# Kernel optimization log

Measured on AMD Instinct MI355X. Metric: run time of the kernel, lower is better.

The kernel has to match this reference:

```python
import jax, jax.numpy as jnp
import numpy as np

IN_C = 64
OUT_C = 128
HEADS = 8
DIM = 9 * IN_C  # 576


def unfold3x3_s2(fea):
    # torch.nn.functional.unfold(fea, (3,3), padding=1, stride=2)
    # returns [N, C*9, L] with channel-major (c, kh, kw) ordering.
    N, C, H, W = fea.shape
    Ho, Wo = H // 2, W // 2
    p = jnp.pad(fea, ((0, 0), (0, 0), (1, 1), (1, 1)))
    patches = jnp.stack(
        [p[:, :, ki:ki + 2 * Ho:2, kj:kj + 2 * Wo:2] for ki in range(3) for kj in range(3)],
        axis=2,
    )  # [N, C, 9, Ho, Wo]
    return patches.reshape(N, C * 9, Ho * Wo)


def mhsa(x, w_qkv, b_qkv, w_out, b_out):
    # standard ViT attention: x [B, L, D]
    B, L, D = x.shape
    dh = D // HEADS
    qkv = x @ w_qkv + b_qkv  # [B, L, 3D]
    q, k, v = jnp.split(qkv, 3, axis=-1)
    def heads(t):
        return t.reshape(B, L, HEADS, dh).transpose(0, 2, 1, 3)  # [B, h, L, dh]
    q, k, v = heads(q), heads(k), heads(v)
    scale = dh ** -0.5
    scores = jnp.einsum('bhqd,bhkd->bhqk', q, k) * scale
    attn = jax.nn.softmax(scores, axis=-1)
    o = jnp.einsum('bhqk,bhkd->bhqd', attn, v)  # [B, h, L, dh]
    o = o.transpose(0, 2, 1, 3).reshape(B, L, D)
    return o @ w_out + b_out


def setup_inputs() -> dict:
    key = jax.random.key(0)
    ks = jax.random.split(key, 6)
    s = DIM ** -0.5
    return {
        'fea': jax.random.normal(ks[0], (1, IN_C, 128, 128), dtype=jnp.float32),
        'w_qkv': jax.random.normal(ks[1], (DIM, 3 * DIM), dtype=jnp.float32) * s,
        'b_qkv': jnp.zeros((3 * DIM,), dtype=jnp.float32),
        'w_out': jax.random.normal(ks[2], (DIM, DIM), dtype=jnp.float32) * s,
        'b_out': jnp.zeros((DIM,), dtype=jnp.float32),
        'conv_w': jax.random.normal(ks[3], (OUT_C, IN_C, 3, 3), dtype=jnp.float32) * s,
    }


def reference(fea, w_qkv, b_qkv, w_out, b_out, conv_w):
    N, C, H, W = fea.shape
    Ho, Wo = H // 2, W // 2
    x = unfold3x3_s2(fea).transpose(0, 2, 1)          # [N, L, 9C]
    x = mhsa(x, w_qkv, b_qkv, w_out, b_out) + x       # residual
    # matmul with reshaped conv weights: [N, L, 9C] @ [9C, out_c]
    y = x @ conv_w.reshape(OUT_C, -1).T               # [N, L, out_c]
    y = y.transpose(0, 2, 1).reshape(N, OUT_C, Ho, Wo)  # fold with (1,1) kernel
    return jax.nn.silu(y)
```

## Files before the change

### kernel.cpp

```cpp
#include <hip/hip_runtime.h>
#include <hip/hip_bf16.h>
#include <math.h>

#define L_TOK 4096
#define D_DIM 576
#define NHEADS 8
#define DHEAD 72
#define DPAD 96
#define HSZ ((size_t)NHEADS * L_TOK * DPAD)
#define KSPLIT 4
#define LOG2E 1.4426950408889634f

typedef __attribute__((ext_vector_type(8))) short short8;
typedef __attribute__((ext_vector_type(4))) short short4v;
typedef __attribute__((ext_vector_type(4))) float float4v;

union F4S8 {
  float4 f4;
  short8 s8;
  __hip_bfloat16 h[8];
};

__device__ inline void tc_body(const float* __restrict__ src,
                               __hip_bfloat16* __restrict__ dst, int R, int C,
                               int bi, int bj, int t, __hip_bfloat16* Ts) {
  const int col = t & 63, row4 = t >> 6;
#pragma unroll
  for (int u = 0; u < 16; u++) {
    int r = u * 4 + row4;
    Ts[r * 68 + col] = __float2bfloat16(src[(size_t)(bj * 64 + r) * C + bi * 64 + col]);
  }
  __syncthreads();
#pragma unroll
  for (int u = 0; u < 16; u++) {
    int c = u * 4 + row4;
    dst[(size_t)(bi * 64 + c) * R + bj * 64 + col] = Ts[col * 68 + c];
  }
}

__global__ __launch_bounds__(256) void prep_all(const float* __restrict__ fea,
                                                const float* __restrict__ w_qkv,
                                                const float* __restrict__ w_out,
                                                const float* __restrict__ conv_w,
                                                __hip_bfloat16* __restrict__ xb,
                                                __hip_bfloat16* __restrict__ WqkvT,
                                                __hip_bfloat16* __restrict__ WoT,
                                                __hip_bfloat16* __restrict__ CwB) {
  __shared__ float Shm[3120];
  const int b = blockIdx.x;
  const int t = threadIdx.x;
  if (b < 512) {
    float* Lf = Shm;
    const int ho = b & 63;
    const int c0 = (b >> 6) * 8;
    for (int e = t; e < 3072; e += 256) {
      int c = e / 384;
      int rr = (e / 128) % 3;
      int w = e & 127;
      int h = 2 * ho + rr - 1;
      float v = 0.f;
      if ((unsigned)h < 128u) v = fea[(size_t)(c0 + c) * 16384 + h * 128 + w];
      Lf[(c * 3 + rr) * 130 + w + 1] = v;
    }
    if (t < 24) { Lf[t * 130] = 0.f; Lf[t * 130 + 129] = 0.f; }
    __syncthreads();
    for (int e = t; e < 576; e += 256) {
      int wo = e / 9, ch = e - wo * 9;
      F4S8 u;
#pragma unroll
      for (int j = 0; j < 8; j++) {
        int dd = ch * 8 + j;
        int c = dd / 9, k = dd - c * 9;
        int ki = k / 3, kj = k - ki * 3;
        u.h[j] = __float2bfloat16(Lf[(c * 3 + ki) * 130 + 2 * wo + kj]);
      }
      *(float4*)(xb + (size_t)(ho * 64 + wo) * D_DIM + c0 * 9 + ch * 8) = u.f4;
    }
  } else if (b < 755) {
    int bb = b - 512;
    tc_body(w_qkv, WqkvT, D_DIM, 1728, bb % 27, bb / 27, t, (__hip_bfloat16*)Shm);
  } else if (b < 836) {
    int bb = b - 755;
    tc_body(w_out, WoT, D_DIM, D_DIM, bb % 9, bb / 9, t, (__hip_bfloat16*)Shm);
  } else {
    int i = (b - 836) * 256 + t;
    CwB[i] = __float2bfloat16(conv_w[i]);
  }
}

template <int EPI, int NMI>
__global__ __launch_bounds__(256) void gemm_mfma(const __hip_bfloat16* __restrict__ A,
                                                 const __hip_bfloat16* __restrict__ Bt,
                                                 const float* __restrict__ bias,
                                                 const __hip_bfloat16* __restrict__ resid,
                                                 __hip_bfloat16* __restrict__ outB,
                                                 __hip_bfloat16* __restrict__ outB2) {
  constexpr int K = D_DIM;
  constexpr int BM = NMI * 32;
  __shared__ __align__(16) __hip_bfloat16 As[BM * 72];
  __shared__ __align__(16) __hip_bfloat16 Bs[64 * 72];
  const int t = threadIdx.x;
  const int wave = t >> 6, lane = t & 63, quad = lane >> 4, l16 = lane & 15;
  const int wm = (wave & 2) * (NMI * 8);
  const int wn = (wave & 1) * 32;
  const int m0 = blockIdx.x * BM, n0 = blockIdx.y * 64;

  float4v acc[NMI][2];
#pragma unroll
  for (int i = 0; i < NMI; i++)
#pragma unroll
    for (int j = 0; j < 2; j++) acc[i][j] = (float4v){0.f, 0.f, 0.f, 0.f};

  const int arow = t >> 3, ach = t & 7;
  for (int k0 = 0; k0 < K; k0 += 64) {
    __syncthreads();
#pragma unroll
    for (int u = 0; u < NMI; u++) {
      int row = u * 32 + arow;
      *(float4*)(&As[row * 72 + ach * 8]) =
          *(const float4*)(A + (size_t)(m0 + row) * K + k0 + ach * 8);
    }
#pragma unroll
    for (int u = 0; u < 2; u++) {
      int row = u * 32 + arow;
      *(float4*)(&Bs[row * 72 + ach * 8]) =
          *(const float4*)(Bt + (size_t)(n0 + row) * K + k0 + ach * 8);
    }
    __syncthreads();
    short8 af[NMI][2], bfr[2][2];
#pragma unroll
    for (int i = 0; i < NMI; i++)
#pragma unroll
      for (int s = 0; s < 2; s++)
        af[i][s] = *(const short8*)(&As[(wm + i * 16 + l16) * 72 + s * 32 + quad * 8]);
#pragma unroll
    for (int j = 0; j < 2; j++)
#pragma unroll
      for (int s = 0; s < 2; s++)
        bfr[j][s] = *(const short8*)(&Bs[(wn + j * 16 + l16) * 72 + s * 32 + quad * 8]);
#pragma unroll
    for (int i = 0; i < NMI; i++)
#pragma unroll
      for (int j = 0; j < 2; j++) {
        acc[i][j] = __builtin_amdgcn_mfma_f32_16x16x32_bf16(af[i][0], bfr[j][0], acc[i][j], 0, 0, 0);
        acc[i][j] = __builtin_amdgcn_mfma_f32_16x16x32_bf16(af[i][1], bfr[j][1], acc[i][j], 0, 0, 0);
      }
  }

  if (EPI == 0) {
    const int part = n0 / D_DIM;
    if (part < 2) {
      __hip_bfloat16* dst = outB + (size_t)part * HSZ;
#pragma unroll
      for (int j = 0; j < 2; j++) {
        int ng = n0 + wn + j * 16 + l16;
        float bv = bias[ng];
        int rem = ng - part * D_DIM;
        int h = rem / DHEAD;
        int d = rem - h * DHEAD;
#pragma unroll
        for (int i = 0; i < NMI; i++) {
          int mb = m0 + wm + i * 16 + quad * 4;
#pragma unroll
          for (int r = 0; r < 4; r++)
            dst[((size_t)h * L_TOK + mb + r) * DPAD + d] = __float2bfloat16(acc[i][j][r] + bv);
        }
      }
    } else {
      __hip_bfloat16* Ls = As;
      __syncthreads();
      const int n0rel = n0 - 2 * D_DIM;
#pragma unroll
      for (int j = 0; j < 2; j++) {
        int nloc = wn + j * 16 + l16;
        float bv = bias[n0 + nloc];
#pragma unroll
        for (int i = 0; i < NMI; i++) {
          int mloc = wm + i * 16 + quad * 4;
#pragma unroll
          for (int r = 0; r < 4; r++)
            Ls[nloc * 136 + mloc + r] = __float2bfloat16(acc[i][j][r] + bv);
        }
      }
      __syncthreads();
      for (int e = t; e < 1024; e += 256) {
        int row = e >> 4, ch = e & 15;
        int ng = n0rel + row;
        int hh = ng / DHEAD, dd = ng - hh * DHEAD;
        *(float4*)(outB2 + ((size_t)hh * DPAD + dd) * L_TOK + m0 + ch * 8) =
            *(const float4*)(&Ls[row * 136 + ch * 8]);
      }
    }
  } else {
#pragma unroll
    for (int j = 0; j < 2; j++) {
      int ng = n0 + wn + j * 16 + l16;
      float bv = bias[ng];
#pragma unroll
      for (int i = 0; i < NMI; i++) {
        int mb = m0 + wm + i * 16 + quad * 4;
#pragma unroll
        for (int r = 0; r < 4; r++) {
          size_t idx = (size_t)(mb + r) * D_DIM + ng;
          float v = acc[i][j][r] + bv + __bfloat162float(resid[idx]);
          outB[idx] = __float2bfloat16(v);
        }
      }
    }
  }
}

__global__ __launch_bounds__(256) void final_small(const __hip_bfloat16* __restrict__ A,
                                                   const __hip_bfloat16* __restrict__ Bt,
                                                   float* __restrict__ out) {
  __shared__ __align__(16) __hip_bfloat16 As[32 * 72];
  __shared__ __align__(16) __hip_bfloat16 Bs[32 * 72];
  const int t = threadIdx.x;
  const int wave = t >> 6, lane = t & 63, quad = lane >> 4, l16 = lane & 15;
  const int wm = (wave & 2) * 8;
  const int wn = (wave & 1) * 16;
  const int m0 = blockIdx.x * 32, n0 = blockIdx.y * 32;

  float4v acc = (float4v){0.f, 0.f, 0.f, 0.f};

  const int arow = t >> 3, ach = t & 7;
  for (int k0 = 0; k0 < D_DIM; k0 += 64) {
    __syncthreads();
    *(float4*)(&As[arow * 72 + ach * 8]) =
        *(const float4*)(A + (size_t)(m0 + arow) * D_DIM + k0 + ach * 8);
    *(float4*)(&Bs[arow * 72 + ach * 8]) =
        *(const float4*)(Bt + (size_t)(n0 + arow) * D_DIM + k0 + ach * 8);
    __syncthreads();
    short8 af[2], bfr[2];
#pragma unroll
    for (int s = 0; s < 2; s++) {
      af[s] = *(const short8*)(&As[(wm + l16) * 72 + s * 32 + quad * 8]);
      bfr[s] = *(const short8*)(&Bs[(wn + l16) * 72 + s * 32 + quad * 8]);
    }
    acc = __builtin_amdgcn_mfma_f32_16x16x32_bf16(af[0], bfr[0], acc, 0, 0, 0);
    acc = __builtin_amdgcn_mfma_f32_16x16x32_bf16(af[1], bfr[1], acc, 0, 0, 0);
  }
  const int oc = n0 + wn + l16;
  const int mb = m0 + wm + quad * 4;
#pragma unroll
  for (int r = 0; r < 4; r++) {
    float v = acc[r];
    float sg = 1.f / (1.f + __expf(-v));
    out[(size_t)oc * L_TOK + mb + r] = v * sg;
  }
}

#define KS_STRIDE 104
#define VT_STRIDE 72
#define PS_STRIDE 72

__global__ __launch_bounds__(256, 2) void attn_mfma(const __hip_bfloat16* __restrict__ Qb,
                                                    const __hip_bfloat16* __restrict__ Kb,
                                                    const __hip_bfloat16* __restrict__ VbT,
                                                    __hip_bfloat16* __restrict__ Opart,
                                                    float* __restrict__ Ml) {
  __shared__ __align__(16) __hip_bfloat16 Ks[64 * KS_STRIDE];
  __shared__ __align__(16) __hip_bfloat16 Vt[80 * VT_STRIDE];
  __shared__ __align__(16) __hip_bfloat16 Ps[4 * 64 * PS_STRIDE];

  const int bid = blockIdx.x;
  const int h = bid & 7;
  const int rest = bid >> 3;
  const int ksp = rest & 3;
  const int qblk = rest >> 2;
  const int t = threadIdx.x;
  const int wave = t >> 6;
  const int lane = t & 63;
  const int quad = lane >> 4;
  const int l16 = lane & 15;

  const __hip_bfloat16* Qh = Qb + (size_t)h * L_TOK * DPAD;
  const __hip_bfloat16* Kh = Kb + (size_t)h * L_TOK * DPAD;
  const __hip_bfloat16* VhT = VbT + (size_t)h * DPAD * L_TOK;

  const int qbase = qblk * 256 + wave * 64;
  short8 qf[4][3];
#pragma unroll
  for (int mi = 0; mi < 4; mi++) {
#pragma unroll
    for (int s = 0; s < 3; s++) {
      if (s == 2 && quad >= 1) {
        qf[mi][s] = (short8){0, 0, 0, 0, 0, 0, 0, 0};
      } else {
        qf[mi][s] = *(const short8*)(Qh + (size_t)(qbase + mi * 16 + l16) * DPAD + s * 32 + quad * 8);
      }
    }
  }

  const float4 zero4 = {0.f, 0.f, 0.f, 0.f};
  if (t < 192) {
    int row = t / 3, ch = 9 + t % 3;
    *(float4*)(&Ks[row * KS_STRIDE + ch * 8]) = zero4;
  }
  if (t >= 192) {
    int e = t - 192;
    int d = 72 + (e >> 3), ch = e & 7;
    *(float4*)(&Vt[d * VT_STRIDE + ch * 8]) = zero4;
  }

  float4v Of[4][5];
#pragma unroll
  for (int mi = 0; mi < 4; mi++)
#pragma unroll
    for (int nt = 0; nt < 5; nt++) Of[mi][nt] = (float4v){0.f, 0.f, 0.f, 0.f};
  float mrow[4] = {-INFINITY, -INFINITY, -INFINITY, -INFINITY};
  float lrow[4] = {0.f, 0.f, 0.f, 0.f};
  const float scale2 = 0.11785113019775792f * LOG2E;

  __hip_bfloat16* myPs = Ps + wave * 64 * PS_STRIDE;
  const int kstart = ksp * 1024;

  for (int kt = 0; kt < 16; kt++) {
    const int kbase = kstart + kt * 64;
    __syncthreads();

    for (int e = t; e < 576; e += 256) {
      int row = e / 9, ch = e - row * 9;
      *(float4*)(&Ks[row * KS_STRIDE + ch * 8]) =
          *(const float4*)(Kh + (size_t)(kbase + row) * DPAD + ch * 8);
    }
    for (int e = t; e < 576; e += 256) {
      int d = e >> 3, ch = e & 7;
      *(float4*)(&Vt[d * VT_STRIDE + ch * 8]) =
          *(const float4*)(VhT + (size_t)d * L_TOK + kbase + ch * 8);
    }
    __syncthreads();

    float4v S[4][4];
#pragma unroll
    for (int ks = 0; ks < 4; ks++) {
      float4v a0 = (float4v){0.f, 0.f, 0.f, 0.f};
      float4v a1 = a0, a2 = a0, a3 = a0;
#pragma unroll
      for (int s = 0; s < 3; s++) {
        short8 kf = *(const short8*)(&Ks[(ks * 16 + l16) * KS_STRIDE + s * 32 + quad * 8]);
        a0 = __builtin_amdgcn_mfma_f32_16x16x32_bf16(kf, qf[0][s], a0, 0, 0, 0);
        a1 = __builtin_amdgcn_mfma_f32_16x16x32_bf16(kf, qf[1][s], a1, 0, 0, 0);
        a2 = __builtin_amdgcn_mfma_f32_16x16x32_bf16(kf, qf[2][s], a2, 0, 0, 0);
        a3 = __builtin_amdgcn_mfma_f32_16x16x32_bf16(kf, qf[3][s], a3, 0, 0, 0);
      }
#pragma unroll
      for (int r = 0; r < 4; r++) {
        S[0][ks][r] = a0[r]; S[1][ks][r] = a1[r];
        S[2][ks][r] = a2[r]; S[3][ks][r] = a3[r];
      }
    }

    float alpha[4];
#pragma unroll
    for (int mi = 0; mi < 4; mi++) {
      float tm = -INFINITY;
#pragma unroll
      for (int ks = 0; ks < 4; ks++)
#pragma unroll
        for (int r = 0; r < 4; r++) tm = fmaxf(tm, S[mi][ks][r]);
      tm = fmaxf(tm, __shfl_xor(tm, 16));
      tm = fmaxf(tm, __shfl_xor(tm, 32));
      float mnew = fmaxf(mrow[mi], tm * scale2);
      alpha[mi] = exp2f(mrow[mi] - mnew);
      mrow[mi] = mnew;
      float ps = 0.f;
#pragma unroll
      for (int ks = 0; ks < 4; ks++)
#pragma unroll
        for (int r = 0; r < 4; r++) {
          float p = exp2f(fmaf(S[mi][ks][r], scale2, -mnew));
          ps += p;
          S[mi][ks][r] = p;
        }
      ps += __shfl_xor(ps, 16);
      ps += __shfl_xor(ps, 32);
      lrow[mi] = lrow[mi] * alpha[mi] + ps;
    }

#pragma unroll
    for (int mi = 0; mi < 4; mi++) {
#pragma unroll
      for (int ks = 0; ks < 4; ks++) {
        union { short4v v; __hip_bfloat16 hh[4]; } pk;
#pragma unroll
        for (int r = 0; r < 4; r++) pk.hh[r] = __float2bfloat16(S[mi][ks][r]);
        *(short4v*)(&myPs[(mi * 16 + l16) * PS_STRIDE + ks * 16 + quad * 4]) = pk.v;
      }
    }

    {
      float aq[4][4];
#pragma unroll
      for (int mi = 0; mi < 4; mi++)
#pragma unroll
        for (int r = 0; r < 4; r++) aq[mi][r] = __shfl(alpha[mi], quad * 4 + r);
#pragma unroll
      for (int mi = 0; mi < 4; mi++)
#pragma unroll
        for (int nt = 0; nt < 5; nt++)
#pragma unroll
          for (int r = 0; r < 4; r++) Of[mi][nt][r] *= aq[mi][r];
    }

#pragma unroll
    for (int kstep = 0; kstep < 2; kstep++) {
      short8 pa[4];
#pragma unroll
      for (int mi = 0; mi < 4; mi++)
        pa[mi] = *(const short8*)(&myPs[(mi * 16 + l16) * PS_STRIDE + kstep * 32 + quad * 8]);
#pragma unroll
      for (int nt = 0; nt < 5; nt++) {
        short8 vb = *(const short8*)(&Vt[(nt * 16 + l16) * VT_STRIDE + kstep * 32 + quad * 8]);
        Of[0][nt] = __builtin_amdgcn_mfma_f32_16x16x32_bf16(pa[0], vb, Of[0][nt], 0, 0, 0);
        Of[1][nt] = __builtin_amdgcn_mfma_f32_16x16x32_bf16(pa[1], vb, Of[1][nt], 0, 0, 0);
        Of[2][nt] = __builtin_amdgcn_mfma_f32_16x16x32_bf16(pa[2], vb, Of[2][nt], 0, 0, 0);
        Of[3][nt] = __builtin_amdgcn_mfma_f32_16x16x32_bf16(pa[3], vb, Of[3][nt], 0, 0, 0);
      }
    }
  }

  const size_t pb = ((size_t)ksp * NHEADS + h) * L_TOK;
#pragma unroll
  for (int mi = 0; mi < 4; mi++) {
#pragma unroll
    for (int nt = 0; nt < 5; nt++) {
      int d = nt * 16 + l16;
      if (d < DHEAD) {
#pragma unroll
        for (int r = 0; r < 4; r++) {
          int q = qbase + mi * 16 + quad * 4 + r;
          Opart[(pb + q) * 72 + d] = __float2bfloat16(Of[mi][nt][r]);
        }
      }
    }
  }
  if (quad == 0) {
#pragma unroll
    for (int mi = 0; mi < 4; mi++) {
      int q = qbase + mi * 16 + l16;
      Ml[(pb + q) * 2] = mrow[mi];
      Ml[(pb + q) * 2 + 1] = lrow[mi];
    }
  }
}

__global__ __launch_bounds__(256) void attn_merge(const __hip_bfloat16* __restrict__ Opart,
                                                  const float* __restrict__ Ml,
                                                  __hip_bfloat16* __restrict__ ob) {
  int idx = blockIdx.x * 256 + threadIdx.x;
  int h = idx / (L_TOK * 9);
  int rem = idx - h * (L_TOK * 9);
  int q = rem / 9;
  int ch = rem - q * 9;
  size_t b[KSPLIT];
  float m[KSPLIT], l[KSPLIT];
  float mx = -INFINITY;
#pragma unroll
  for (int s = 0; s < KSPLIT; s++) {
    b[s] = ((size_t)s * NHEADS + h) * L_TOK + q;
    m[s] = Ml[b[s] * 2];
    l[s] = Ml[b[s] * 2 + 1];
    mx = fmaxf(mx, m[s]);
  }
  float w[KSPLIT], denom = 0.f;
#pragma unroll
  for (int s = 0; s < KSPLIT; s++) {
    w[s] = exp2f(m[s] - mx);
    denom += w[s] * l[s];
  }
  float inv = 1.f / denom;
  float acc[8] = {0, 0, 0, 0, 0, 0, 0, 0};
#pragma unroll
  for (int s = 0; s < KSPLIT; s++) {
    short8 o = *(const short8*)(Opart + b[s] * 72 + ch * 8);
#pragma unroll
    for (int j = 0; j < 8; j++) {
      union { short ss; __hip_bfloat16 bb; } u;
      u.ss = o[j];
      acc[j] += w[s] * __bfloat162float(u.bb);
    }
  }
  __hip_bfloat16* dst = ob + (size_t)q * D_DIM + h * DHEAD + ch * 8;
#pragma unroll
  for (int j = 0; j < 8; j++) dst[j] = __float2bfloat16(acc[j] * inv);
}

extern "C" void kernel_launch(void* const* d_in, const int* in_sizes, int n_in,
                              void* d_out, int out_size, void* d_ws, size_t ws_size,
                              hipStream_t stream) {
  const float* fea    = (const float*)d_in[0];
  const float* w_qkv  = (const float*)d_in[1];
  const float* b_qkv  = (const float*)d_in[2];
  const float* w_out  = (const float*)d_in[3];
  const float* b_out  = (const float*)d_in[4];
  const float* conv_w = (const float*)d_in[5];
  float* out = (float*)d_out;

  __hip_bfloat16* xb    = (__hip_bfloat16*)d_ws;
  __hip_bfloat16* WqkvT = xb + (size_t)L_TOK * D_DIM;
  __hip_bfloat16* WoT   = WqkvT + (size_t)1728 * D_DIM;
  __hip_bfloat16* CwB   = WoT + (size_t)D_DIM * D_DIM;
  __hip_bfloat16* QKb   = CwB + (size_t)128 * D_DIM;
  __hip_bfloat16* VbT   = QKb + 2 * HSZ;
  __hip_bfloat16* Opart = VbT + HSZ;
  float* Ml = (float*)(Opart + (size_t)KSPLIT * NHEADS * L_TOK * 72);
  __hip_bfloat16* ob = QKb;
  __hip_bfloat16* xr = Opart;

  prep_all<<<1124, 256, 0, stream>>>(fea, w_qkv, w_out, conv_w, xb, WqkvT, WoT, CwB);
  gemm_mfma<0, 4><<<dim3(32, 27), 256, 0, stream>>>(xb, WqkvT, b_qkv, nullptr, QKb, VbT);
  attn_mfma<<<512, 256, 0, stream>>>(QKb, QKb + HSZ, VbT, Opart, Ml);
  attn_merge<<<1152, 256, 0, stream>>>(Opart, Ml, ob);
  gemm_mfma<1, 2><<<dim3(64, 9), 256, 0, stream>>>(ob, WoT, b_out, xb, xr, nullptr);
  final_small<<<dim3(128, 4), 256, 0, stream>>>(xr, CwB, out);
}
```

Measured before the change: 203.7 us.

## Double-buffer K/V tiles in attention and halve the P scratch buffer

The attention kernel now keeps two LDS buffers for the K and V^T tiles. The next tile is staged while the current one is computed, so there is one barrier per iteration instead of two. The bf16 P tile is written to LDS in two 32-column halves, each just before its PV MFMA step, which shrinks the per-wave P scratch stride. This costs extra LDS for the second K/V buffer, and the global loads are still synchronous, so how much latency is hidden depends on how the compiler schedules them.

Result: no change. 202.2 us (-0.7%).

```diff
diff --git a/kernel.cpp b/kernel.cpp
--- a/kernel.cpp
+++ b/kernel.cpp
@@ -252,15 +252,17 @@
 
 #define KS_STRIDE 104
 #define VT_STRIDE 72
-#define PS_STRIDE 72
+#define PS_STRIDE 40
+#define KBUF (64 * KS_STRIDE)
+#define VBUF (80 * VT_STRIDE)
 
 __global__ __launch_bounds__(256, 2) void attn_mfma(const __hip_bfloat16* __restrict__ Qb,
                                                     const __hip_bfloat16* __restrict__ Kb,
                                                     const __hip_bfloat16* __restrict__ VbT,
                                                     __hip_bfloat16* __restrict__ Opart,
                                                     float* __restrict__ Ml) {
-  __shared__ __align__(16) __hip_bfloat16 Ks[64 * KS_STRIDE];
-  __shared__ __align__(16) __hip_bfloat16 Vt[80 * VT_STRIDE];
+  __shared__ __align__(16) __hip_bfloat16 Ks[2 * KBUF];
+  __shared__ __align__(16) __hip_bfloat16 Vt[2 * VBUF];
   __shared__ __align__(16) __hip_bfloat16 Ps[4 * 64 * PS_STRIDE];
 
   const int bid = blockIdx.x;
@@ -296,11 +298,12 @@
   if (t < 192) {
     int row = t / 3, ch = 9 + t % 3;
     *(float4*)(&Ks[row * KS_STRIDE + ch * 8]) = zero4;
-  }
-  if (t >= 192) {
+    *(float4*)(&Ks[KBUF + row * KS_STRIDE + ch * 8]) = zero4;
+  } else {
     int e = t - 192;
     int d = 72 + (e >> 3), ch = e & 7;
     *(float4*)(&Vt[d * VT_STRIDE + ch * 8]) = zero4;
+    *(float4*)(&Vt[VBUF + d * VT_STRIDE + ch * 8]) = zero4;
   }
 
   float4v Of[4][5];
@@ -315,21 +318,29 @@
   __hip_bfloat16* myPs = Ps + wave * 64 * PS_STRIDE;
   const int kstart = ksp * 1024;
 
-  for (int kt = 0; kt < 16; kt++) {
-    const int kbase = kstart + kt * 64;
-    __syncthreads();
-
+  auto stage = [&](int kbase, __hip_bfloat16* Kw, __hip_bfloat16* Vw) {
     for (int e = t; e < 576; e += 256) {
       int row = e / 9, ch = e - row * 9;
-      *(float4*)(&Ks[row * KS_STRIDE + ch * 8]) =
+      *(float4*)(&Kw[row * KS_STRIDE + ch * 8]) =
           *(const float4*)(Kh + (size_t)(kbase + row) * DPAD + ch * 8);
     }
     for (int e = t; e < 576; e += 256) {
       int d = e >> 3, ch = e & 7;
-      *(float4*)(&Vt[d * VT_STRIDE + ch * 8]) =
+      *(float4*)(&Vw[d * VT_STRIDE + ch * 8]) =
           *(const float4*)(VhT + (size_t)d * L_TOK + kbase + ch * 8);
     }
-    __syncthreads();
+  };
+
+  stage(kstart, Ks, Vt);
+  __syncthreads();
+
+  for (int kt = 0; kt < 16; kt++) {
+    const int p = kt & 1;
+    if (kt + 1 < 16)
+      stage(kstart + (kt + 1) * 64, Ks + (1 - p) * KBUF, Vt + (1 - p) * VBUF);
+
+    const __hip_bfloat16* Ksb = Ks + p * KBUF;
+    const __hip_bfloat16* Vtb = Vt + p * VBUF;
 
     float4v S[4][4];
 #pragma unroll
@@ -338,7 +349,7 @@
       float4v a1 = a0, a2 = a0, a3 = a0;
 #pragma unroll
       for (int s = 0; s < 3; s++) {
-        short8 kf = *(const short8*)(&Ks[(ks * 16 + l16) * KS_STRIDE + s * 32 + quad * 8]);
+        short8 kf = *(const short8*)(&Ksb[(ks * 16 + l16) * KS_STRIDE + s * 32 + quad * 8]);
         a0 = __builtin_amdgcn_mfma_f32_16x16x32_bf16(kf, qf[0][s], a0, 0, 0, 0);
         a1 = __builtin_amdgcn_mfma_f32_16x16x32_bf16(kf, qf[1][s], a1, 0, 0, 0);
         a2 = __builtin_amdgcn_mfma_f32_16x16x32_bf16(kf, qf[2][s], a2, 0, 0, 0);
@@ -369,26 +380,15 @@
       for (int ks = 0; ks < 4; ks++)
 #pragma unroll
         for (int r = 0; r < 4; r++) {
-          float p = exp2f(fmaf(S[mi][ks][r], scale2, -mnew));
-          ps += p;
-          S[mi][ks][r] = p;
+          float p2 = exp2f(fmaf(S[mi][ks][r], scale2, -mnew));
+          ps += p2;
+          S[mi][ks][r] = p2;
         }
       ps += __shfl_xor(ps, 16);
       ps += __shfl_xor(ps, 32);
       lrow[mi] = lrow[mi] * alpha[mi] + ps;
     }
 
-#pragma unroll
-    for (int mi = 0; mi < 4; mi++) {
-#pragma unroll
-      for (int ks = 0; ks < 4; ks++) {
-        union { short4v v; __hip_bfloat16 hh[4]; } pk;
-#pragma unroll
-        for (int r = 0; r < 4; r++) pk.hh[r] = __float2bfloat16(S[mi][ks][r]);
-        *(short4v*)(&myPs[(mi * 16 + l16) * PS_STRIDE + ks * 16 + quad * 4]) = pk.v;
-      }
-    }
-
     {
       float aq[4][4];
 #pragma unroll
@@ -405,19 +405,32 @@
 
 #pragma unroll
     for (int kstep = 0; kstep < 2; kstep++) {
+#pragma unroll
+      for (int mi = 0; mi < 4; mi++) {
+#pragma unroll
+        for (int k2 = 0; k2 < 2; k2++) {
+          int ks = kstep * 2 + k2;
+          union { short4v v; __hip_bfloat16 hh[4]; } pk;
+#pragma unroll
+          for (int r = 0; r < 4; r++) pk.hh[r] = __float2bfloat16(S[mi][ks][r]);
+          *(short4v*)(&myPs[(mi * 16 + l16) * PS_STRIDE + k2 * 16 + quad * 4]) = pk.v;
+        }
+      }
       short8 pa[4];
 #pragma unroll
       for (int mi = 0; mi < 4; mi++)
-        pa[mi] = *(const short8*)(&myPs[(mi * 16 + l16) * PS_STRIDE + kstep * 32 + quad * 8]);
+        pa[mi] = *(const short8*)(&myPs[(mi * 16 + l16) * PS_STRIDE + quad * 8]);
 #pragma unroll
       for (int nt = 0; nt < 5; nt++) {
-        short8 vb = *(const short8*)(&Vt[(nt * 16 + l16) * VT_STRIDE + kstep * 32 + quad * 8]);
+        short8 vb = *(const short8*)(&Vtb[(nt * 16 + l16) * VT_STRIDE + kstep * 32 + quad * 8]);
         Of[0][nt] = __builtin_amdgcn_mfma_f32_16x16x32_bf16(pa[0], vb, Of[0][nt], 0, 0, 0);
         Of[1][nt] = __builtin_amdgcn_mfma_f32_16x16x32_bf16(pa[1], vb, Of[1][nt], 0, 0, 0);
         Of[2][nt] = __builtin_amdgcn_mfma_f32_16x16x32_bf16(pa[2], vb, Of[2][nt], 0, 0, 0);
         Of[3][nt] = __builtin_amdgcn_mfma_f32_16x16x32_bf16(pa[3], vb, Of[3][nt], 0, 0, 0);
       }
     }
+
+    __syncthreads();
   }
 
   const size_t pb = ((size_t)ksp * NHEADS + h) * L_TOK;
```
